# Kernel tuning notes

Hardware: AMD Instinct MI355X
Metric: run time of the kernel (lower is better)

The kernel has to match this reference:

```python
import jax, jax.numpy as jnp
import numpy as np

N = 50000
E = 800000
D_IN = 128
D_OUT = 128
K = 3


def setup_inputs() -> dict:
    key = jax.random.key(0)
    k1, k2, k3, k4, k5 = jax.random.split(key, 5)
    x = jax.random.normal(k1, (N, D_IN), dtype=jnp.float32)
    TT = jax.random.uniform(k2, (E, K), dtype=jnp.float32)
    weight = jax.random.normal(k3, (D_IN, D_OUT, K), dtype=jnp.float32) * 0.1
    bias = jax.random.normal(k4, (D_OUT,), dtype=jnp.float32) * 0.1
    edge_idx = jax.random.randint(k5, (2, E), 0, N, dtype=jnp.int64)
    return {"x": x, "TT": TT, "weight": weight, "bias": bias, "edge_idx": edge_idx}


def reference(x, TT, weight, bias, edge_idx):
    # out = sum_k A_k @ (x @ W[:, :, k]) + bias, A_k sparse COO with values TT[:, k]
    n = x.shape[0]
    row, col = edge_idx[0], edge_idx[1]
    out = jnp.zeros((n, weight.shape[1]), dtype=x.dtype)
    for k in range(weight.shape[2]):  # small fixed kernel count
        support = x @ weight[:, :, k]                 # [N, out]
        msg = TT[:, k, None] * support[col]           # [E, out] gather + scale
        out = out + jax.ops.segment_sum(msg, row, num_segments=n)
    return out + bias
```

## Files before the change

kernel.cpp:

```cpp
#include <hip/hip_runtime.h>
#include <hip/hip_fp16.h>

#define DIM 128
#define KK 3
#define RPB 16
#define ZPAD 392
#define EBLK 4096
#define NBKT 256
#define CAPB 5120
#define QF   384
#define OVF_CAP 65536

typedef __attribute__((ext_vector_type(4))) float f32x4;
typedef __attribute__((ext_vector_type(2))) float f32x2;
typedef __attribute__((ext_vector_type(8))) short bf16x8;
typedef __attribute__((ext_vector_type(4))) unsigned int u32x4;

__device__ __forceinline__ void nt_store16(uint4* p, uint4 v) {
    u32x4 t = {v.x, v.y, v.z, v.w};
    __builtin_nontemporal_store(t, (u32x4*)p);
}
__device__ __forceinline__ uint4 nt_load16(const uint4* p) {
    u32x4 t = __builtin_nontemporal_load((const u32x4*)p);
    return make_uint4(t[0], t[1], t[2], t[3]);
}

__device__ __forceinline__ unsigned pkbf(float lo, float hi) {
    unsigned a = __float_as_uint(lo), b = __float_as_uint(hi);
    a = (a + 0x7fffu + ((a >> 16) & 1u)) >> 16;
    b = (b + 0x7fffu + ((b >> 16) & 1u)) & 0xffff0000u;
    return (a & 0xffffu) | b;
}

__device__ __forceinline__ void wave_scan256(const int* cnt, int* scn, int tid) {
    if (tid < 64) {
        int v0 = cnt[tid * 4 + 0], v1 = cnt[tid * 4 + 1];
        int v2 = cnt[tid * 4 + 2], v3 = cnt[tid * 4 + 3];
        int s4 = v0 + v1 + v2 + v3;
        int inc = s4;
#pragma unroll
        for (int d = 1; d < 64; d <<= 1) {
            int t = __shfl_up(inc, d);
            if (tid >= d) inc += t;
        }
        int ex = inc - s4;
        scn[tid * 4 + 0] = ex;
        scn[tid * 4 + 1] = ex + v0;
        scn[tid * 4 + 2] = ex + v0 + v1;
        scn[tid * 4 + 3] = ex + v0 + v1 + v2;
    }
}

__global__ __launch_bounds__(1024) void prep_kernel(
        const float* __restrict__ x, const float* __restrict__ w,
        const float* __restrict__ TT, const int* __restrict__ eidx,
        uint2* __restrict__ xb2q, bf16x8* __restrict__ wbf,
        int* __restrict__ bucketCnt, uint4* __restrict__ rec16,
        int* __restrict__ ovf_cnt, uint4* __restrict__ ovf,
        int xq_total, int xblk, int E) {
    __shared__ unsigned sw0[EBLK], sw1[EBLK], sw2[EBLK], sw3[EBLK];
    __shared__ int hist[NBKT], scn[NBKT], cursor[NBKT], gbase[NBKT];
    int tid = threadIdx.x, b = blockIdx.x;

    if (b < xblk) {
        int i = b * 1024 + tid;
        if (i < xq_total) {
            float4 v = ((const float4*)x)[i];
            xb2q[i] = make_uint2(pkbf(v.x, v.y), pkbf(v.z, v.w));
        }
        return;
    }
    if (b < xblk + 6) {
        int t = (b - xblk) * 1024 + tid;
        if (t < 12 * 8 * 64) {
            int lane = t & 63;
            int quad = lane >> 4;
            int nn = ((t >> 6) & 7) * 16 + (lane & 15);
            int kbase = (t >> 9) * 32 + quad * 8;
            short vals[8];
#pragma unroll
            for (int j = 0; j < 8; ++j) {
                int k = kbase + j;
                int k3 = k >> 7, i2 = k & (DIM - 1);
                unsigned bv = __float_as_uint(w[((size_t)i2 * DIM + nn) * KK + k3]);
                vals[j] = (short)((bv + 0x7fffu + ((bv >> 16) & 1u)) >> 16);
            }
            wbf[t] = *(const bf16x8*)vals;
        }
        return;
    }

    int e0 = (b - xblk - 6) * EBLK;
    int nval = min(EBLK, E - e0);

    if (tid < NBKT) hist[tid] = 0;
    __syncthreads();

    unsigned w0v[4], w1v[4], w2v[4], w3v[4];
    int bv[4];
#pragma unroll
    for (int i = 0; i < 4; ++i) {
        int li = tid + i * 1024;
        bv[i] = -1;
        if (li < nval) {
            int e = e0 + li;
            int row = eidx[e];
            int col = eidx[(size_t)E + e];
            w0v[i] = (unsigned)col | ((unsigned)row << 16);
            w1v[i] = __float_as_uint(TT[(size_t)e * 3 + 0]);
            w2v[i] = __float_as_uint(TT[(size_t)e * 3 + 1]);
            w3v[i] = __float_as_uint(TT[(size_t)e * 3 + 2]);
            bv[i] = row >> 8;
            atomicAdd(&hist[bv[i]], 1);
        }
    }
    __syncthreads();

    wave_scan256(hist, scn, tid);
    __syncthreads();
    if (tid < NBKT) {
        cursor[tid] = scn[tid];
        gbase[tid] = atomicAdd(&bucketCnt[tid], hist[tid]);
    }
    __syncthreads();

#pragma unroll
    for (int i = 0; i < 4; ++i) {
        if (bv[i] >= 0) {
            int lpos = atomicAdd(&cursor[bv[i]], 1);
            sw0[lpos] = w0v[i]; sw1[lpos] = w1v[i];
            sw2[lpos] = w2v[i]; sw3[lpos] = w3v[i];
        }
    }
    __syncthreads();

    for (int s = tid; s < nval; s += 1024) {
        unsigned u0 = sw0[s];
        int bb = (int)(u0 >> 24);
        int gpos = gbase[bb] + (s - scn[bb]);
        if (gpos < CAPB) {
            nt_store16(&rec16[(size_t)bb * CAPB + gpos],
                       make_uint4(u0, sw1[s], sw2[s], sw3[s]));
        } else {
            int op = atomicAdd(ovf_cnt, 1);
            if (op < OVF_CAP)
                ovf[op] = make_uint4(u0, sw1[s], sw2[s], sw3[s]);
        }
    }
}

__global__ __launch_bounds__(1024) void binB_kernel(
        const uint4* __restrict__ rec16, const int* __restrict__ bucketCnt,
        uint4* __restrict__ out16, int* __restrict__ rowStart,
        int* __restrict__ rowCnt) {
    __shared__ uint4 ostage[CAPB];
    __shared__ int hist[256], scn[256], cursor[256];
    int b = blockIdx.x, tid = threadIdx.x;
    int cntb = min(bucketCnt[b], CAPB);

    if (tid < 256) hist[tid] = 0;
    __syncthreads();
    for (int i = tid; i < cntb; i += 1024) {
        unsigned u0 = rec16[(size_t)b * CAPB + i].x;
        atomicAdd(&hist[(u0 >> 16) & 255u], 1);
    }
    __syncthreads();
    wave_scan256(hist, scn, tid);
    __syncthreads();
    if (tid < 256) {
        cursor[tid] = scn[tid];
        rowStart[b * 256 + tid] = b * CAPB + scn[tid];
        rowCnt[b * 256 + tid] = hist[tid];
    }
    __syncthreads();
    for (int i = tid; i < cntb; i += 1024) {
        uint4 r = rec16[(size_t)b * CAPB + i];
        int rl = (int)((r.x >> 16) & 255u);
        int pos = atomicAdd(&cursor[rl], 1);
        ostage[pos] = r;
    }
    __syncthreads();
    for (int i = tid; i < cntb; i += 1024)
        nt_store16(&out16[(size_t)b * CAPB + i], ostage[i]);
}

__device__ __forceinline__ void edge_fma(uint4 rc, const unsigned* __restrict__ xb2,
        int lane, f32x2& A0, f32x2& A1, f32x2& A2) {
    int c = rc.x & 0xffffu;
    unsigned u = xb2[(size_t)c * 64 + lane];
    f32x2 xv;
    xv.x = __uint_as_float(u << 16);
    xv.y = __uint_as_float(u & 0xffff0000u);
    float t0 = __uint_as_float(rc.y);
    float t1 = __uint_as_float(rc.z);
    float t2 = __uint_as_float(rc.w);
#if __has_builtin(__builtin_elementwise_fma)
    A0 = __builtin_elementwise_fma((f32x2){t0, t0}, xv, A0);
    A1 = __builtin_elementwise_fma((f32x2){t1, t1}, xv, A1);
    A2 = __builtin_elementwise_fma((f32x2){t2, t2}, xv, A2);
#else
    A0.x = fmaf(t0, xv.x, A0.x); A0.y = fmaf(t0, xv.y, A0.y);
    A1.x = fmaf(t1, xv.x, A1.x); A1.y = fmaf(t1, xv.y, A1.y);
    A2.x = fmaf(t2, xv.x, A2.x); A2.y = fmaf(t2, xv.y, A2.y);
#endif
}

__global__ __launch_bounds__(256) void fused_kernel(const uint4* __restrict__ out16,
        const int* __restrict__ rowStart, const int* __restrict__ rowCnt,
        const unsigned* __restrict__ xb2, const bf16x8* __restrict__ wbf,
        const float* __restrict__ bias, float* __restrict__ out,
        int* __restrict__ ovf_cnt, uint4* __restrict__ ovf, int n) {
    __shared__ short zs16[RPB][ZPAD];
    __shared__ uint4 qflat[QF];
    __shared__ int rs[RPB], rc[RPB];
    int tid = threadIdx.x;
    int lane = tid & 63, wv = tid >> 6;
    int n0 = blockIdx.x * RPB;

    if (tid < RPB) {
        int r = n0 + tid;
        rs[tid] = (r < n) ? rowStart[r] : 0;
        rc[tid] = (r < n) ? rowCnt[r] : 0;
    }
    __syncthreads();
    int base = rs[0];
    int tot = rs[RPB - 1] + rc[RPB - 1] - base;

    for (int i = tid; i < tot; i += 256) {
        uint4 r = nt_load16(&out16[(size_t)base + i]);
        if (i < QF) qflat[i] = r;
        else {
            int op = atomicAdd(ovf_cnt, 1);
            if (op < OVF_CAP) ovf[op] = r;
        }
    }
    __syncthreads();

#pragma unroll
    for (int ii = 0; ii < 4; ++ii) {
        int rl = wv * 4 + ii;
        f32x2 A0 = {0.f, 0.f}, A1 = {0.f, 0.f}, A2 = {0.f, 0.f};
        int s = min(rs[rl] - base, QF);
        int hi = min(rs[rl] - base + rc[rl], QF);
        int p = s;
        for (; p + 4 <= hi; p += 4) {
            uint4 r0 = qflat[p], r1 = qflat[p + 1], r2 = qflat[p + 2], r3 = qflat[p + 3];
            edge_fma(r0, xb2, lane, A0, A1, A2);
            edge_fma(r1, xb2, lane, A0, A1, A2);
            edge_fma(r2, xb2, lane, A0, A1, A2);
            edge_fma(r3, xb2, lane, A0, A1, A2);
        }
        for (; p < hi; ++p)
            edge_fma(qflat[p], xb2, lane, A0, A1, A2);
        *(unsigned*)&zs16[rl][0 * DIM + 2 * lane] = pkbf(A0.x, A0.y);
        *(unsigned*)&zs16[rl][1 * DIM + 2 * lane] = pkbf(A1.x, A1.y);
        *(unsigned*)&zs16[rl][2 * DIM + 2 * lane] = pkbf(A2.x, A2.y);
    }
    __syncthreads();

    int quad = lane >> 4, m = lane & 15;
    int nt0 = wv * 2, nt1 = wv * 2 + 1;
    f32x4 acc0 = {0.f, 0.f, 0.f, 0.f}, acc1 = {0.f, 0.f, 0.f, 0.f};
#pragma unroll
    for (int kt = 0; kt < 12; ++kt) {
        bf16x8 a  = *(const bf16x8*)&zs16[m][kt * 32 + quad * 8];
        bf16x8 b0 = wbf[(kt * 8 + nt0) * 64 + lane];
        bf16x8 b1 = wbf[(kt * 8 + nt1) * 64 + lane];
        acc0 = __builtin_amdgcn_mfma_f32_16x16x32_bf16(a, b0, acc0, 0, 0, 0);
        acc1 = __builtin_amdgcn_mfma_f32_16x16x32_bf16(a, b1, acc1, 0, 0, 0);
    }
    float bi0 = bias[nt0 * 16 + m], bi1 = bias[nt1 * 16 + m];
#pragma unroll
    for (int rr = 0; rr < 4; ++rr) {
        int node = n0 + quad * 4 + rr;
        if (node < n) {
            __builtin_nontemporal_store(acc0[rr] + bi0,
                &out[(size_t)node * DIM + nt0 * 16 + m]);
            __builtin_nontemporal_store(acc1[rr] + bi1,
                &out[(size_t)node * DIM + nt1 * 16 + m]);
        }
    }
}

__global__ __launch_bounds__(128) void ovf_kernel(const uint4* __restrict__ ovf,
        const int* __restrict__ ovf_cnt, const float* __restrict__ x,
        const float* __restrict__ w, float* __restrict__ out) {
    int total = min(*ovf_cnt, OVF_CAP);
    int d = threadIdx.x;
    for (int i = blockIdx.x; i < total; i += gridDim.x) {
        uint4 r = ovf[i];
        int col = (int)(r.x & 0xffffu), row = (int)(r.x >> 16);
        float t0 = __uint_as_float(r.y);
        float t1 = __uint_as_float(r.z);
        float t2 = __uint_as_float(r.w);
        float acc = 0.f;
        for (int ii = 0; ii < DIM; ++ii) {
            const float* wp = &w[((size_t)ii * DIM + d) * KK];
            acc = fmaf(x[(size_t)col * DIM + ii],
                       t0 * wp[0] + t1 * wp[1] + t2 * wp[2], acc);
        }
        atomicAdd(&out[(size_t)row * DIM + d], acc);
    }
}

extern "C" void kernel_launch(void* const* d_in, const int* in_sizes, int n_in,
                              void* d_out, int out_size, void* d_ws, size_t ws_size,
                              hipStream_t stream) {
    const float* x    = (const float*)d_in[0];
    const float* TT   = (const float*)d_in[1];
    const float* w    = (const float*)d_in[2];
    const float* bias = (const float*)d_in[3];
    const int*   eidx = (const int*)d_in[4];
    float* out = (float*)d_out;

    int n = in_sizes[0] / DIM;
    int E = in_sizes[1] / KK;
    int nbkt = (n + 255) >> 8;
    int ntiles = (n + RPB - 1) / RPB;

    char* ws = (char*)d_ws;
    size_t o = 0;
    auto take = [&](size_t b) { void* p = ws + o; o += (b + 255) & ~(size_t)255; return p; };
    uint4*    rec16 = (uint4*)take((size_t)nbkt * CAPB * 16);
    uint4*    out16 = (uint4*)take((size_t)nbkt * CAPB * 16);
    int*      rowStart = (int*)take((size_t)nbkt * 256 * 4);
    int*      rowCnt   = (int*)take((size_t)nbkt * 256 * 4);
    int*      bcnt  = (int*)take((size_t)(NBKT + 64) * 4);
    uint4*    ovf   = (uint4*)take((size_t)OVF_CAP * 16);
    bf16x8*   wbf   = (bf16x8*)take((size_t)12 * 8 * 64 * 16);
    unsigned* xb2   = (unsigned*)take((size_t)n * DIM * 2);
    (void)ws_size;
    int* ovf_cnt = bcnt + NBKT;

    hipMemsetAsync(bcnt, 0, (size_t)(NBKT + 64) * 4, stream);

    int xq = n * DIM / 4;
    int xblk = (xq + 1023) / 1024;
    int ablk = (E + EBLK - 1) / EBLK;

    prep_kernel<<<xblk + 6 + ablk, 1024, 0, stream>>>(
        x, w, TT, eidx, (uint2*)xb2, wbf, bcnt, rec16, ovf_cnt, ovf, xq, xblk, E);
    binB_kernel<<<nbkt, 1024, 0, stream>>>(rec16, bcnt, out16, rowStart, rowCnt);
    fused_kernel<<<ntiles, 256, 0, stream>>>(
        out16, rowStart, rowCnt, xb2, wbf, bias, out, ovf_cnt, ovf, n);
    ovf_kernel<<<64, 128, 0, stream>>>(ovf, ovf_cnt, x, w, out);
}
```

Baseline: 148.4 us.

## Vectorize edge loads, pack LDS staging, fold overflow handling into fused kernel

The prep kernel now loads each thread's four consecutive edges with int4/float4 loads and stages records in a single uint4 shared array instead of four scalar arrays. The fused kernel no longer spills staging overflow to a global list; it reads excess edges straight from global memory and scans the prep-stage overflow list per row. This lets the separate overflow kernel launch be dropped. The cost is that every fused block reads ovf_cnt and loops over the overflow list, which is cheap only when the list is empty.

```diff
diff --git a/kernel.cpp b/kernel.cpp
--- a/kernel.cpp
+++ b/kernel.cpp
@@ -58,7 +58,7 @@
         int* __restrict__ bucketCnt, uint4* __restrict__ rec16,
         int* __restrict__ ovf_cnt, uint4* __restrict__ ovf,
         int xq_total, int xblk, int E) {
-    __shared__ unsigned sw0[EBLK], sw1[EBLK], sw2[EBLK], sw3[EBLK];
+    __shared__ uint4 sw4[EBLK];
     __shared__ int hist[NBKT], scn[NBKT], cursor[NBKT], gbase[NBKT];
     int tid = threadIdx.x, b = blockIdx.x;
 
@@ -98,20 +98,39 @@
 
     unsigned w0v[4], w1v[4], w2v[4], w3v[4];
     int bv[4];
-#pragma unroll
-    for (int i = 0; i < 4; ++i) {
-        int li = tid + i * 1024;
-        bv[i] = -1;
-        if (li < nval) {
-            int e = e0 + li;
-            int row = eidx[e];
-            int col = eidx[(size_t)E + e];
-            w0v[i] = (unsigned)col | ((unsigned)row << 16);
-            w1v[i] = __float_as_uint(TT[(size_t)e * 3 + 0]);
-            w2v[i] = __float_as_uint(TT[(size_t)e * 3 + 1]);
-            w3v[i] = __float_as_uint(TT[(size_t)e * 3 + 2]);
-            bv[i] = row >> 8;
-            atomicAdd(&hist[bv[i]], 1);
+    int t4 = tid * 4;
+    if (t4 + 4 <= nval && ((E & 3) == 0)) {
+        int4 rw = *(const int4*)&eidx[(size_t)e0 + t4];
+        int4 cl = *(const int4*)&eidx[(size_t)E + e0 + t4];
+        const float4* tp = (const float4*)(TT + (size_t)(e0 + t4) * 3);
+        float4 ta = tp[0], tb = tp[1], tc = tp[2];
+        w0v[0] = (unsigned)cl.x | ((unsigned)rw.x << 16);
+        w0v[1] = (unsigned)cl.y | ((unsigned)rw.y << 16);
+        w0v[2] = (unsigned)cl.z | ((unsigned)rw.z << 16);
+        w0v[3] = (unsigned)cl.w | ((unsigned)rw.w << 16);
+        w1v[0] = __float_as_uint(ta.x); w2v[0] = __float_as_uint(ta.y); w3v[0] = __float_as_uint(ta.z);
+        w1v[1] = __float_as_uint(ta.w); w2v[1] = __float_as_uint(tb.x); w3v[1] = __float_as_uint(tb.y);
+        w1v[2] = __float_as_uint(tb.z); w2v[2] = __float_as_uint(tb.w); w3v[2] = __float_as_uint(tc.x);
+        w1v[3] = __float_as_uint(tc.y); w2v[3] = __float_as_uint(tc.z); w3v[3] = __float_as_uint(tc.w);
+        bv[0] = rw.x >> 8; bv[1] = rw.y >> 8; bv[2] = rw.z >> 8; bv[3] = rw.w >> 8;
+#pragma unroll
+        for (int i = 0; i < 4; ++i) atomicAdd(&hist[bv[i]], 1);
+    } else {
+#pragma unroll
+        for (int i = 0; i < 4; ++i) {
+            int li = t4 + i;
+            bv[i] = -1;
+            if (li < nval) {
+                int e = e0 + li;
+                int row = eidx[e];
+                int col = eidx[(size_t)E + e];
+                w0v[i] = (unsigned)col | ((unsigned)row << 16);
+                w1v[i] = __float_as_uint(TT[(size_t)e * 3 + 0]);
+                w2v[i] = __float_as_uint(TT[(size_t)e * 3 + 1]);
+                w3v[i] = __float_as_uint(TT[(size_t)e * 3 + 2]);
+                bv[i] = row >> 8;
+                atomicAdd(&hist[bv[i]], 1);
+            }
         }
     }
     __syncthreads();
@@ -128,23 +147,20 @@
     for (int i = 0; i < 4; ++i) {
         if (bv[i] >= 0) {
             int lpos = atomicAdd(&cursor[bv[i]], 1);
-            sw0[lpos] = w0v[i]; sw1[lpos] = w1v[i];
-            sw2[lpos] = w2v[i]; sw3[lpos] = w3v[i];
+            sw4[lpos] = make_uint4(w0v[i], w1v[i], w2v[i], w3v[i]);
         }
     }
     __syncthreads();
 
     for (int s = tid; s < nval; s += 1024) {
-        unsigned u0 = sw0[s];
-        int bb = (int)(u0 >> 24);
+        uint4 r = sw4[s];
+        int bb = (int)(r.x >> 24);
         int gpos = gbase[bb] + (s - scn[bb]);
         if (gpos < CAPB) {
-            nt_store16(&rec16[(size_t)bb * CAPB + gpos],
-                       make_uint4(u0, sw1[s], sw2[s], sw3[s]));
+            nt_store16(&rec16[(size_t)bb * CAPB + gpos], r);
         } else {
             int op = atomicAdd(ovf_cnt, 1);
-            if (op < OVF_CAP)
-                ovf[op] = make_uint4(u0, sw1[s], sw2[s], sw3[s]);
+            if (op < OVF_CAP) ovf[op] = r;
         }
     }
 }
@@ -209,7 +225,7 @@
         const int* __restrict__ rowStart, const int* __restrict__ rowCnt,
         const unsigned* __restrict__ xb2, const bf16x8* __restrict__ wbf,
         const float* __restrict__ bias, float* __restrict__ out,
-        int* __restrict__ ovf_cnt, uint4* __restrict__ ovf, int n) {
+        const int* __restrict__ ovf_cnt, const uint4* __restrict__ ovf, int n) {
     __shared__ short zs16[RPB][ZPAD];
     __shared__ uint4 qflat[QF];
     __shared__ int rs[RPB], rc[RPB];
@@ -225,24 +241,21 @@
     __syncthreads();
     int base = rs[0];
     int tot = rs[RPB - 1] + rc[RPB - 1] - base;
-
-    for (int i = tid; i < tot; i += 256) {
-        uint4 r = nt_load16(&out16[(size_t)base + i]);
-        if (i < QF) qflat[i] = r;
-        else {
-            int op = atomicAdd(ovf_cnt, 1);
-            if (op < OVF_CAP) ovf[op] = r;
-        }
-    }
+    int tovf = min(*ovf_cnt, OVF_CAP);
+
+    int stg = min(tot, QF);
+    for (int i = tid; i < stg; i += 256)
+        qflat[i] = nt_load16(&out16[(size_t)base + i]);
     __syncthreads();
 
 #pragma unroll
     for (int ii = 0; ii < 4; ++ii) {
         int rl = wv * 4 + ii;
         f32x2 A0 = {0.f, 0.f}, A1 = {0.f, 0.f}, A2 = {0.f, 0.f};
-        int s = min(rs[rl] - base, QF);
-        int hi = min(rs[rl] - base + rc[rl], QF);
-        int p = s;
+        int s_gl = rs[rl] - base;
+        int e_gl = s_gl + rc[rl];
+        int p = min(s_gl, QF);
+        int hi = min(e_gl, QF);
         for (; p + 4 <= hi; p += 4) {
             uint4 r0 = qflat[p], r1 = qflat[p + 1], r2 = qflat[p + 2], r3 = qflat[p + 3];
             edge_fma(r0, xb2, lane, A0, A1, A2);
@@ -252,6 +265,13 @@
         }
         for (; p < hi; ++p)
             edge_fma(qflat[p], xb2, lane, A0, A1, A2);
+        for (int q = max(s_gl, QF); q < e_gl; ++q)
+            edge_fma(out16[(size_t)base + q], xb2, lane, A0, A1, A2);
+        for (int oi = 0; oi < tovf; ++oi) {
+            uint4 r = ovf[oi];
+            if ((int)(r.x >> 16) == n0 + rl)
+                edge_fma(r, xb2, lane, A0, A1, A2);
+        }
         *(unsigned*)&zs16[rl][0 * DIM + 2 * lane] = pkbf(A0.x, A0.y);
         *(unsigned*)&zs16[rl][1 * DIM + 2 * lane] = pkbf(A1.x, A1.y);
         *(unsigned*)&zs16[rl][2 * DIM + 2 * lane] = pkbf(A2.x, A2.y);
@@ -279,27 +299,6 @@
             __builtin_nontemporal_store(acc1[rr] + bi1,
                 &out[(size_t)node * DIM + nt1 * 16 + m]);
         }
-    }
-}
-
-__global__ __launch_bounds__(128) void ovf_kernel(const uint4* __restrict__ ovf,
-        const int* __restrict__ ovf_cnt, const float* __restrict__ x,
-        const float* __restrict__ w, float* __restrict__ out) {
-    int total = min(*ovf_cnt, OVF_CAP);
-    int d = threadIdx.x;
-    for (int i = blockIdx.x; i < total; i += gridDim.x) {
-        uint4 r = ovf[i];
-        int col = (int)(r.x & 0xffffu), row = (int)(r.x >> 16);
-        float t0 = __uint_as_float(r.y);
-        float t1 = __uint_as_float(r.z);
-        float t2 = __uint_as_float(r.w);
-        float acc = 0.f;
-        for (int ii = 0; ii < DIM; ++ii) {
-            const float* wp = &w[((size_t)ii * DIM + d) * KK];
-            acc = fmaf(x[(size_t)col * DIM + ii],
-                       t0 * wp[0] + t1 * wp[1] + t2 * wp[2], acc);
-        }
-        atomicAdd(&out[(size_t)row * DIM + d], acc);
     }
 }
 
@@ -343,5 +342,4 @@
     binB_kernel<<<nbkt, 1024, 0, stream>>>(rec16, bcnt, out16, rowStart, rowCnt);
     fused_kernel<<<ntiles, 256, 0, stream>>>(
         out16, rowStart, rowCnt, xb2, wbf, bias, out, ovf_cnt, ovf, n);
-    ovf_kernel<<<64, 128, 0, stream>>>(ovf, ovf_cnt, x, w, out);
-}
+}
```

New measurement: 148.1 us. No clear change (-0.2%).
